# Kernel tuning notes

Measured on AMD Instinct MI355X. Metric: run time of the kernel, lower is better.

The kernel has to match this reference:

```python
import jax, jax.numpy as jnp
import numpy as np

NUM_HEADS = 16
KERNEL_SIZE = 13


def setup_inputs() -> dict:
    key = jax.random.key(0)
    ks = jax.random.split(key, 6)
    B, L, C = 4, 4096, 512
    H, K = NUM_HEADS, KERNEL_SIZE
    x = jax.random.normal(ks[0], (B, L, C), dtype=jnp.float32)
    qkv_w = jax.random.normal(ks[1], (C, 3 * C), dtype=jnp.float32) * 0.02
    qkv_b = jnp.zeros((3 * C,), dtype=jnp.float32)
    rpb = jax.random.normal(ks[2], (H, 2 * K - 1), dtype=jnp.float32) * 0.02
    proj_w = jax.random.normal(ks[3], (C, C), dtype=jnp.float32) * 0.02
    proj_b = jnp.zeros((C,), dtype=jnp.float32)
    return {"x": x, "qkv_w": qkv_w, "qkv_b": qkv_b, "rpb": rpb,
            "proj_w": proj_w, "proj_b": proj_b}


def reference(x, qkv_w, qkv_b, rpb, proj_w, proj_b):
    B, L, C = x.shape
    H, K = NUM_HEADS, KERNEL_SIZE
    hd = C // H
    scale = hd ** -0.5
    kh = K // 2

    # qkv projection -> q,k,v each [B,H,L,hd]
    qkv = (x @ qkv_w + qkv_b).reshape(B, L, 3, H, hd).transpose(2, 0, 3, 1, 4)
    q, k, v = qkv[0] * scale, qkv[1], qkv[2]

    # NATTEN window: start index clamped so window stays in-bounds
    pos = jnp.arange(L)
    ni = jnp.clip(pos - kh, 0, L - K)              # [L] window start per query
    idx = ni[:, None] + jnp.arange(K)[None, :]     # [L,K] key positions
    # rpb index: (key_pos - query_pos) + (K-1)
    rpb_idx = (ni - pos + (K - 1))[:, None] + jnp.arange(K)[None, :]  # [L,K]

    k_win = k[:, :, idx, :]                        # [B,H,L,K,hd]
    v_win = v[:, :, idx, :]                        # [B,H,L,K,hd]

    attn = jnp.einsum('bhld,bhlkd->bhlk', q, k_win) + rpb[:, rpb_idx][None]
    attn = jax.nn.softmax(attn, axis=-1)

    out = jnp.einsum('bhlk,bhlkd->bhld', attn, v_win)  # [B,H,L,hd]
    out = out.transpose(0, 2, 1, 3).reshape(B, L, C)
    return out @ proj_w + proj_b
```

## Files before the change

kernel.cpp:

```cpp
#include <hip/hip_runtime.h>
#include <hip/hip_bf16.h>
#include <stdint.h>


typedef __attribute__((ext_vector_type(8))) short short8;
typedef __attribute__((ext_vector_type(4))) float f32x4;
typedef __attribute__((ext_vector_type(8))) unsigned short u16x8;
typedef __attribute__((ext_vector_type(4))) float float4v;

#define NB 4
#define NL 4096
#define NC 512
#define NH 16
#define HD 32
#define KW 13
#define KHALF 6
#define NM (NB*NL)

__device__ __forceinline__ float b2f(unsigned short u) {
  union { unsigned int i; float f; } x; x.i = ((unsigned int)u) << 16; return x.f;
}
__device__ __forceinline__ unsigned short f2b(float f) {
  __hip_bfloat16 h = __float2bfloat16(f);
  return __builtin_bit_cast(unsigned short, h);
}
__device__ __forceinline__ void gll16(const unsigned short* g, unsigned short* l) {
  __builtin_amdgcn_global_load_lds(
      (const __attribute__((address_space(1))) void*)g,
      (__attribute__((address_space(3))) void*)l, 16, 0, 0);
}

__global__ __launch_bounds__(256) void cvt_f32_bf16(const float* __restrict__ in,
                                                    unsigned short* __restrict__ out) {
  long i = (long)blockIdx.x * 256 + threadIdx.x;
  const float4v* in4 = (const float4v*)in;
  float4v a = in4[i * 2];
  float4v b = in4[i * 2 + 1];
  u16x8 u;
  u[0] = f2b(a.x); u[1] = f2b(a.y); u[2] = f2b(a.z); u[3] = f2b(a.w);
  u[4] = f2b(b.x); u[5] = f2b(b.y); u[6] = f2b(b.z); u[7] = f2b(b.w);
  ((u16x8*)out)[i] = u;
}

__global__ __launch_bounds__(256) void transpose_bf16(const float* __restrict__ in,
                                                      unsigned short* __restrict__ out,
                                                      int R, int C) {
  __shared__ float t[32][33];
  int c0 = blockIdx.x * 32;
  int r0 = blockIdx.y * 32;
  int tx = threadIdx.x;
  int ty = threadIdx.y;
  #pragma unroll
  for (int i = ty; i < 32; i += 8)
    t[i][tx] = in[(long)(r0 + i) * C + c0 + tx];
  __syncthreads();
  #pragma unroll
  for (int i = ty; i < 32; i += 8)
    out[(long)(c0 + i) * R + r0 + tx] = f2b(t[tx][i]);
}


__device__ __forceinline__ void stage_tile(const unsigned short* __restrict__ G,
                                           long rowBase, int K, int kt,
                                           unsigned short* ldsDst, int tid) {
  int r  = tid >> 3;
  int ch = (tid & 7) ^ (r & 7);
  const unsigned short* s0 = G + (rowBase + r) * (long)K + kt * 64 + ch * 8;
  unsigned short* d0 = ldsDst + tid * 8;
  #pragma unroll
  for (int q = 0; q < 4; ++q)
    gll16(s0 + (long)32 * q * K, d0 + 2048 * q);
}

#define BAR() __builtin_amdgcn_s_barrier()
#define LGK0() do { asm volatile("s_waitcnt lgkmcnt(0)" ::: "memory"); \
                    __builtin_amdgcn_sched_barrier(0); } while (0)
#define VM(N) asm volatile("s_waitcnt vmcnt(" #N ")" ::: "memory")

#define LDA(ABASE) do { \
  const char* _ba = (const char*)(ABASE); \
  _Pragma("unroll") for (int ii = 0; ii < 4; ++ii) { \
    int _row = wm*64 + ii*16 + lr; \
    _Pragma("unroll") for (int kb = 0; kb < 2; ++kb) \
      af[ii][kb] = *(const short8*)(_ba + _row*128 + (((kb*4+lk) ^ lr7) * 16)); \
  } \
} while (0)

#define LDB(BBASE) do { \
  const char* _bb = (const char*)(BBASE); \
  _Pragma("unroll") for (int jj = 0; jj < 4; ++jj) { \
    int _row = wn*64 + jj*16 + lr; \
    _Pragma("unroll") for (int kb = 0; kb < 2; ++kb) \
      bf[jj][kb] = *(const short8*)(_bb + _row*128 + (((kb*4+lk) ^ lr7) * 16)); \
  } \
} while (0)

#define MMA_ALL() do { \
  __builtin_amdgcn_s_setprio(1); \
  _Pragma("unroll") for (int ii = 0; ii < 4; ++ii) \
    _Pragma("unroll") for (int jj = 0; jj < 4; ++jj) \
      _Pragma("unroll") for (int kb = 0; kb < 2; ++kb) \
        acc[ii][jj] = __builtin_amdgcn_mfma_f32_16x16x32_bf16( \
            af[ii][kb], bf[jj][kb], acc[ii][jj], 0, 0, 0); \
  __builtin_amdgcn_s_setprio(0); \
} while (0)

#define KTILE(AB, BB, KT, STG, VMARG) do { \
  LDA(AB); LDB(BB); LGK0(); \
  BAR(); \
  if (STG) { \
    stage_tile(Ag, mBase, K, (KT) + 2, AB, tid); \
    stage_tile(Bg, nBase, K, (KT) + 2, BB, tid); \
  } \
  MMA_ALL(); \
  VMARG; \
  BAR(); \
} while (0)

template<int OUT_BF16>
__global__ __launch_bounds__(256, 2)
void gemm128(const unsigned short* __restrict__ Ag,
             const unsigned short* __restrict__ Bg,
             const float* __restrict__ bias,
             void* __restrict__ Cout,
             int M, int N, int K, int tilesN) {
  __shared__ __align__(16) unsigned short lds[32768];

  int tid = threadIdx.x;
  int nwg = gridDim.x;
  int cpx = nwg >> 3;
  int wg  = ((int)blockIdx.x & 7) * cpx + ((int)blockIdx.x >> 3);
  int tm = wg / tilesN, tn = wg % tilesN;
  long mBase = (long)tm * 128;
  long nBase = (long)tn * 128;

  int lane = tid & 63, wave = tid >> 6;
  int wm = wave >> 1;
  int wn = wave & 1;
  int lr = lane & 15, lk = lane >> 4, lr7 = lr & 7;

  unsigned short* A0 = lds;
  unsigned short* A1 = lds + 8192;
  unsigned short* B0 = lds + 16384;
  unsigned short* B1 = lds + 24576;

  f32x4 acc[4][4];
  #pragma unroll
  for (int i = 0; i < 4; ++i)
    #pragma unroll
    for (int j = 0; j < 4; ++j) acc[i][j] = (f32x4){0.f, 0.f, 0.f, 0.f};

  short8 af[4][2], bf[4][2];

  stage_tile(Ag, mBase, K, 0, A0, tid);
  stage_tile(Bg, nBase, K, 0, B0, tid);
  stage_tile(Ag, mBase, K, 1, A1, tid);
  stage_tile(Bg, nBase, K, 1, B1, tid);
  VM(8);
  BAR();

  #pragma unroll 1
  for (int i = 0; i < 4; ++i) {
    int kt = 2 * i;
    if (i < 3) {
      KTILE(A0, B0, kt,     true,  VM(8));
      KTILE(A1, B1, kt + 1, true,  VM(8));
    } else {
      KTILE(A0, B0, kt,     false, VM(0));
      KTILE(A1, B1, kt + 1, false, (void)0);
    }
  }

  long rowb = mBase + wm * 64 + (lane >> 4) * 4;
  int  colb = (int)nBase + wn * 64 + lr;
  if (OUT_BF16) {
    unsigned short* C = (unsigned short*)Cout;
    #pragma unroll
    for (int mi = 0; mi < 4; ++mi)
      #pragma unroll
      for (int nj = 0; nj < 4; ++nj) {
        int col = colb + nj * 16;
        float bv = bias[col];
        #pragma unroll
        for (int r = 0; r < 4; ++r)
          C[(rowb + mi * 16 + r) * (long)N + col] = f2b(acc[mi][nj][r] + bv);
      }
  } else {
    float* C = (float*)Cout;
    #pragma unroll
    for (int mi = 0; mi < 4; ++mi)
      #pragma unroll
      for (int nj = 0; nj < 4; ++nj) {
        int col = colb + nj * 16;
        float bv = bias[col];
        #pragma unroll
        for (int r = 0; r < 4; ++r)
          C[(rowb + mi * 16 + r) * (long)N + col] = acc[mi][nj][r] + bv;
      }
  }
}

__global__ __launch_bounds__(256)
void natt(const unsigned short* __restrict__ qkv, const float* __restrict__ rpb,
          unsigned short* __restrict__ out) {
  int tid = blockIdx.x * 256 + threadIdx.x;
  int h = tid & 15;
  int l = (tid >> 4) & (NL - 1);
  int b = tid >> 16;
  const float scale = 0.17677669529663687f;

  long qb = ((long)(b * NL + l) * 3) * NC + h * HD;
  float q[HD];
  {
    const u16x8* q8 = (const u16x8*)(qkv + qb);
    #pragma unroll
    for (int w = 0; w < 4; ++w) {
      u16x8 u = q8[w];
      #pragma unroll
      for (int e = 0; e < 8; ++e) q[w * 8 + e] = b2f(u[e]) * scale;
    }
  }

  int ni = l - KHALF;
  if (ni < 0) ni = 0;
  if (ni > NL - KW) ni = NL - KW;
  const float* rb = rpb + h * (2 * KW - 1) + (ni - l + KW - 1);

  float p[KW];
  float mx = -1e30f;
  #pragma unroll
  for (int j = 0; j < KW; ++j) {
    long kb = ((long)(b * NL + ni + j) * 3 + 1) * NC + h * HD;
    const u16x8* k8 = (const u16x8*)(qkv + kb);
    float s = 0.f;
    #pragma unroll
    for (int w = 0; w < 4; ++w) {
      u16x8 u = k8[w];
      #pragma unroll
      for (int e = 0; e < 8; ++e) s += q[w * 8 + e] * b2f(u[e]);
    }
    s += rb[j];
    p[j] = s;
    mx = fmaxf(mx, s);
  }

  float sum = 0.f;
  #pragma unroll
  for (int j = 0; j < KW; ++j) { p[j] = __expf(p[j] - mx); sum += p[j]; }
  float inv = 1.0f / sum;

  float o[HD];
  #pragma unroll
  for (int d = 0; d < HD; ++d) o[d] = 0.f;
  #pragma unroll
  for (int j = 0; j < KW; ++j) {
    long vb = ((long)(b * NL + ni + j) * 3 + 2) * NC + h * HD;
    const u16x8* v8 = (const u16x8*)(qkv + vb);
    float wj = p[j] * inv;
    #pragma unroll
    for (int w = 0; w < 4; ++w) {
      u16x8 u = v8[w];
      #pragma unroll
      for (int e = 0; e < 8; ++e) o[w * 8 + e] += wj * b2f(u[e]);
    }
  }

  unsigned short* op = out + (long)(b * NL + l) * NC + h * HD;
  #pragma unroll
  for (int w = 0; w < 4; ++w) {
    u16x8 u;
    #pragma unroll
    for (int e = 0; e < 8; ++e) u[e] = f2b(o[w * 8 + e]);
    *((u16x8*)(op + w * 8)) = u;
  }
}

extern "C" void kernel_launch(void* const* d_in, const int* in_sizes, int n_in,
                              void* d_out, int out_size, void* d_ws, size_t ws_size,
                              hipStream_t stream) {
  const float* x      = (const float*)d_in[0];
  const float* qkv_w  = (const float*)d_in[1];
  const float* qkv_b  = (const float*)d_in[2];
  const float* rpb    = (const float*)d_in[3];
  const float* proj_w = (const float*)d_in[4];
  const float* proj_b = (const float*)d_in[5];
  float* out = (float*)d_out;

  char* ws = (char*)d_ws;
  unsigned short* xb     = (unsigned short*)(ws);
  unsigned short* qkvwT  = (unsigned short*)(ws + 16777216);
  unsigned short* projwT = (unsigned short*)(ws + 18350080);
  unsigned short* qkvo   = (unsigned short*)(ws + 18874368);
  unsigned short* attno  = (unsigned short*)(ws + 69206016);

  cvt_f32_bf16<<<dim3(4096), dim3(256), 0, stream>>>(x, xb);
  transpose_bf16<<<dim3(48, 16), dim3(32, 8), 0, stream>>>(qkv_w, qkvwT, 512, 1536);
  transpose_bf16<<<dim3(16, 16), dim3(32, 8), 0, stream>>>(proj_w, projwT, 512, 512);
  gemm128<1><<<dim3(1536), dim3(256), 0, stream>>>(xb, qkvwT, qkv_b, qkvo,
                                                   NM, 1536, 512, 12);
  natt<<<dim3(1024), dim3(256), 0, stream>>>(qkvo, rpb, attno);
  gemm128<0><<<dim3(512), dim3(256), 0, stream>>>(attno, projwT, proj_b, out,
                                                  NM, 512, 512, 4);
}
```

Baseline: 101.6 us.

## Pre-pack weights into MFMA fragment layout and load B directly from global

Replaces the weight transpose with a packing kernel that writes the B operand in exact per-lane MFMA fragment order. The GEMM then loads B fragments straight from global memory (likely L2-resident) instead of staging them through LDS. This halves LDS use and raises the occupancy hint to 3 workgroups per CU. The trade-off is global-load latency on the B path with no LDS reuse between the two wave rows, plus a reordered vmcnt wait placed before the MFMAs.

```diff
diff --git a/kernel.cpp b/kernel.cpp
--- a/kernel.cpp
+++ b/kernel.cpp
@@ -42,27 +42,29 @@
   ((u16x8*)out)[i] = u;
 }
 
-__global__ __launch_bounds__(256) void transpose_bf16(const float* __restrict__ in,
-                                                      unsigned short* __restrict__ out,
-                                                      int R, int C) {
-  __shared__ float t[32][33];
-  int c0 = blockIdx.x * 32;
-  int r0 = blockIdx.y * 32;
-  int tx = threadIdx.x;
-  int ty = threadIdx.y;
-  #pragma unroll
-  for (int i = ty; i < 32; i += 8)
-    t[i][tx] = in[(long)(r0 + i) * C + c0 + tx];
-  __syncthreads();
-  #pragma unroll
-  for (int i = ty; i < 32; i += 8)
-    out[(long)(c0 + i) * R + r0 + tx] = f2b(t[tx][i]);
-}
-
-
-__device__ __forceinline__ void stage_tile(const unsigned short* __restrict__ G,
-                                           long rowBase, int K, int kt,
-                                           unsigned short* ldsDst, int tid) {
+__global__ __launch_bounds__(256)
+void pack_bf(const float* __restrict__ W, unsigned short* __restrict__ Bf,
+             int N, int ngroups) {
+  int g = blockIdx.x * 256 + threadIdx.x;
+  if (g >= ngroups) return;
+  int lane = g & 63;
+  int kb   = (g >> 6) & 1;
+  int nj   = (g >> 7) & 3;
+  int wn   = (g >> 9) & 1;
+  int kt   = (g >> 10) & 7;
+  int tn   = g >> 13;
+  int n  = tn * 128 + wn * 64 + nj * 16 + (lane & 15);
+  int k0 = kt * 64 + (kb * 4 + (lane >> 4)) * 8;
+  u16x8 u;
+  #pragma unroll
+  for (int e = 0; e < 8; ++e) u[e] = f2b(W[(long)(k0 + e) * N + n]);
+  ((u16x8*)Bf)[g] = u;
+}
+
+
+__device__ __forceinline__ void stage_tileA(const unsigned short* __restrict__ G,
+                                            long rowBase, int K, int kt,
+                                            unsigned short* ldsDst, int tid) {
   int r  = tid >> 3;
   int ch = (tid & 7) ^ (r & 7);
   const unsigned short* s0 = G + (rowBase + r) * (long)K + kt * 64 + ch * 8;
@@ -86,13 +88,11 @@
   } \
 } while (0)
 
-#define LDB(BBASE) do { \
-  const char* _bb = (const char*)(BBASE); \
-  _Pragma("unroll") for (int jj = 0; jj < 4; ++jj) { \
-    int _row = wn*64 + jj*16 + lr; \
+#define LDBG(KT) do { \
+  const short8* _bp = (const short8*)(Bfw + (long)(KT) * 8192) + lane; \
+  _Pragma("unroll") for (int nj = 0; nj < 4; ++nj) \
     _Pragma("unroll") for (int kb = 0; kb < 2; ++kb) \
-      bf[jj][kb] = *(const short8*)(_bb + _row*128 + (((kb*4+lk) ^ lr7) * 16)); \
-  } \
+      bf[nj][kb] = _bp[(nj*2 + kb) * 64]; \
 } while (0)
 
 #define MMA_ALL() do { \
@@ -105,26 +105,25 @@
   __builtin_amdgcn_s_setprio(0); \
 } while (0)
 
-#define KTILE(AB, BB, KT, STG, VMARG) do { \
-  LDA(AB); LDB(BB); LGK0(); \
+#define GTILE(ABUF, KT, STG, VMARG) do { \
+  LDBG(KT); \
+  LDA(ABUF); \
+  LGK0(); \
   BAR(); \
-  if (STG) { \
-    stage_tile(Ag, mBase, K, (KT) + 2, AB, tid); \
-    stage_tile(Bg, nBase, K, (KT) + 2, BB, tid); \
-  } \
+  if (STG) stage_tileA(Ag, mBase, K, (KT) + 2, ABUF, tid); \
+  VMARG; \
   MMA_ALL(); \
-  VMARG; \
   BAR(); \
 } while (0)
 
 template<int OUT_BF16>
-__global__ __launch_bounds__(256, 2)
+__global__ __launch_bounds__(256, 3)
 void gemm128(const unsigned short* __restrict__ Ag,
-             const unsigned short* __restrict__ Bg,
+             const unsigned short* __restrict__ Bf,
              const float* __restrict__ bias,
              void* __restrict__ Cout,
              int M, int N, int K, int tilesN) {
-  __shared__ __align__(16) unsigned short lds[32768];
+  __shared__ __align__(16) unsigned short lds[16384];
 
   int tid = threadIdx.x;
   int nwg = gridDim.x;
@@ -139,10 +138,10 @@
   int wn = wave & 1;
   int lr = lane & 15, lk = lane >> 4, lr7 = lr & 7;
 
+  const unsigned short* Bfw = Bf + (long)tn * 65536 + wn * 4096;
+
   unsigned short* A0 = lds;
   unsigned short* A1 = lds + 8192;
-  unsigned short* B0 = lds + 16384;
-  unsigned short* B1 = lds + 24576;
 
   f32x4 acc[4][4];
   #pragma unroll
@@ -152,24 +151,18 @@
 
   short8 af[4][2], bf[4][2];
 
-  stage_tile(Ag, mBase, K, 0, A0, tid);
-  stage_tile(Bg, nBase, K, 0, B0, tid);
-  stage_tile(Ag, mBase, K, 1, A1, tid);
-  stage_tile(Bg, nBase, K, 1, B1, tid);
-  VM(8);
+  stage_tileA(Ag, mBase, K, 0, A0, tid);
+  stage_tileA(Ag, mBase, K, 1, A1, tid);
+  VM(4);
   BAR();
 
   #pragma unroll 1
-  for (int i = 0; i < 4; ++i) {
-    int kt = 2 * i;
-    if (i < 3) {
-      KTILE(A0, B0, kt,     true,  VM(8));
-      KTILE(A1, B1, kt + 1, true,  VM(8));
-    } else {
-      KTILE(A0, B0, kt,     false, VM(0));
-      KTILE(A1, B1, kt + 1, false, (void)0);
-    }
-  }
+  for (int i = 0; i < 3; ++i) {
+    GTILE(A0, 2*i,     true, VM(4));
+    GTILE(A1, 2*i + 1, true, VM(4));
+  }
+  GTILE(A0, 6, false, VM(0));
+  GTILE(A1, 7, false, VM(0));
 
   long rowb = mBase + wm * 64 + (lane >> 4) * 4;
   int  colb = (int)nBase + wn * 64 + lr;
@@ -287,18 +280,18 @@
   float* out = (float*)d_out;
 
   char* ws = (char*)d_ws;
-  unsigned short* xb     = (unsigned short*)(ws);
-  unsigned short* qkvwT  = (unsigned short*)(ws + 16777216);
-  unsigned short* projwT = (unsigned short*)(ws + 18350080);
-  unsigned short* qkvo   = (unsigned short*)(ws + 18874368);
-  unsigned short* attno  = (unsigned short*)(ws + 69206016);
+  unsigned short* xb   = (unsigned short*)(ws);
+  unsigned short* Bf1  = (unsigned short*)(ws + 16777216);
+  unsigned short* Bf2  = (unsigned short*)(ws + 18350080);
+  unsigned short* qkvo = (unsigned short*)(ws + 18874368);
+  unsigned short* attno= (unsigned short*)(ws + 69206016);
 
   cvt_f32_bf16<<<dim3(4096), dim3(256), 0, stream>>>(x, xb);
-  transpose_bf16<<<dim3(48, 16), dim3(32, 8), 0, stream>>>(qkv_w, qkvwT, 512, 1536);
-  transpose_bf16<<<dim3(16, 16), dim3(32, 8), 0, stream>>>(proj_w, projwT, 512, 512);
-  gemm128<1><<<dim3(1536), dim3(256), 0, stream>>>(xb, qkvwT, qkv_b, qkvo,
+  pack_bf<<<dim3(384), dim3(256), 0, stream>>>(qkv_w, Bf1, 1536, 98304);
+  pack_bf<<<dim3(128), dim3(256), 0, stream>>>(proj_w, Bf2, 512, 32768);
+  gemm128<1><<<dim3(1536), dim3(256), 0, stream>>>(xb, Bf1, qkv_b, qkvo,
                                                    NM, 1536, 512, 12);
   natt<<<dim3(1024), dim3(256), 0, stream>>>(qkvo, rpb, attno);
-  gemm128<0><<<dim3(512), dim3(256), 0, stream>>>(attno, projwT, proj_b, out,
+  gemm128<0><<<dim3(512), dim3(256), 0, stream>>>(attno, Bf2, proj_b, out,
                                                   NM, 512, 512, 4);
 }
```

Result: faster. 97.41 us (-4.1%).
